# Performance work log

Hardware: AMD Instinct MI355X
Metric: run time of the kernel (lower is better)

Reference implementation:

```python
import jax, jax.numpy as jnp
import numpy as np

E, TWO_I, H = 8, 3072, 2048
I = TWO_I // 2
T = 16384

def setup_inputs() -> dict:
    key = jax.random.key(0)
    k1, k2, k3 = jax.random.split(key, 3)
    scale_gu = 1.0 / np.sqrt(H)
    scale_dn = 1.0 / np.sqrt(I)
    return {
        "current_state": jax.random.normal(k1, (T, H), dtype=jnp.float32),
        "gate_up_proj": jax.random.normal(k2, (E, TWO_I, H), dtype=jnp.float32) * scale_gu,
        "down_proj": jax.random.normal(k3, (E, H, I), dtype=jnp.float32) * scale_dn,
        "expert_idx": 3,
    }

def reference(current_state, gate_up_proj, down_proj, expert_idx):
    # F.linear(x, W) == x @ W.T
    w_gu = gate_up_proj[expert_idx]            # [2I, H]
    w_dn = down_proj[expert_idx]               # [H, I]
    gu = jnp.einsum("th,ih->ti", current_state, w_gu)  # [T, 2I]
    gate, up = jnp.split(gu, 2, axis=-1)       # each [T, I]
    hidden = jax.nn.silu(gate) * up            # SwiGLU gating
    return jnp.einsum("ti,hi->th", hidden, w_dn)  # [T, H]
```

## Files before the change

### kernel.cpp

```cpp
#include <hip/hip_runtime.h>
#include <hip/hip_bf16.h>


namespace {

constexpr int T_ = 16384;
constexpr int H_ = 2048;
constexpr int I_ = 1536;

typedef short short8 __attribute__((ext_vector_type(8)));
typedef float f32x4 __attribute__((ext_vector_type(4)));
typedef unsigned short ushort4v __attribute__((ext_vector_type(4)));

__device__ __forceinline__ unsigned short f2bf(float f) {
    union { float f; unsigned u; } v; v.f = f;
    return (unsigned short)((v.u + 0x7FFFu + ((v.u >> 16) & 1u)) >> 16);
}

typedef __attribute__((address_space(1))) const void gvoid;
typedef __attribute__((address_space(3))) void lvoid;
__device__ __forceinline__ void gload16(const void* g, void* l) {
    __builtin_amdgcn_global_load_lds((gvoid*)g, (lvoid*)l, 16, 0, 0);
}

__global__ void k_cvt_all(const float* __restrict__ x, const float* __restrict__ wgu,
                          const float* __restrict__ wdn, const int* __restrict__ eidx,
                          unsigned short* __restrict__ xb, unsigned short* __restrict__ wgub,
                          unsigned short* __restrict__ wdnb) {
    const int e = *eidx;
    const int n1 = T_ * H_ / 4;
    const int n2 = 2 * I_ * H_ / 4;
    const int n3 = H_ * I_ / 4;
    const int ntot = n1 + n2 + n3;
    const float* wgu_e = wgu + (size_t)e * (size_t)(2 * I_) * H_;
    const float* wdn_e = wdn + (size_t)e * (size_t)H_ * I_;
    const int stride = gridDim.x * blockDim.x;
    for (int i = blockIdx.x * blockDim.x + threadIdx.x; i < ntot; i += stride) {
        const float* src; unsigned short* dst; int j;
        if (i < n1)           { src = x;     dst = xb;   j = i; }
        else if (i < n1 + n2) { src = wgu_e; dst = wgub; j = i - n1; }
        else                  { src = wdn_e; dst = wdnb; j = i - n1 - n2; }
        f32x4 v = ((const f32x4*)src)[j];
        ushort4v h = { f2bf(v[0]), f2bf(v[1]), f2bf(v[2]), f2bf(v[3]) };
        ((ushort4v*)dst)[j] = h;
    }
}

__global__ __launch_bounds__(256, 2) void k_gemm1_swiglu(
    const unsigned short* __restrict__ xb, const unsigned short* __restrict__ wgub,
    unsigned short* __restrict__ hidden)
{
    __shared__ unsigned short lds[3 * 128 * 64];
    unsigned short* ldsA  = lds;
    unsigned short* ldsBg = lds + 128 * 64;
    unsigned short* ldsBu = lds + 2 * 128 * 64;

    const int tid  = threadIdx.x;
    const int lane = tid & 63;
    const int wv   = tid >> 6;
    const int wr   = wv >> 1, wc = wv & 1;

    const int nb = (blockIdx.x & 7) * 192 + (blockIdx.x >> 3);
    const int bx = nb % 12, by = nb / 12;
    const int m0 = by * 128;
    const int n0 = bx * 128;

    f32x4 accG[4][4], accU[4][4];
    #pragma unroll
    for (int a = 0; a < 4; ++a)
        #pragma unroll
        for (int b = 0; b < 4; ++b) { accG[a][b] = (f32x4)0.0f; accU[a][b] = (f32x4)0.0f; }

    const int drow = lane >> 3;
    const int gcol = (((lane & 7) ^ drow) * 8);
    const int l15 = lane & 15;
    const int l4  = lane >> 4;
    const int sw  = l15 & 7;

    for (int k0 = 0; k0 < H_; k0 += 64) {
        __syncthreads();
        #pragma unroll
        for (int r = 0; r < 4; ++r) {
            const int row  = r * 32 + wv * 8 + drow;
            const int loff = r * 2048 + wv * 512;
            gload16(xb   + (size_t)(m0 + row)      * H_ + k0 + gcol, ldsA  + loff);
            gload16(wgub + (size_t)(n0 + row)      * H_ + k0 + gcol, ldsBg + loff);
            gload16(wgub + (size_t)(I_ + n0 + row) * H_ + k0 + gcol, ldsBu + loff);
        }
        __syncthreads();

        #pragma unroll
        for (int kk = 0; kk < 2; ++kk) {
            const int sl = ((kk * 4 + l4) ^ sw) * 8;
            short8 af[4], bg[4], bu[4];
            #pragma unroll
            for (int a = 0; a < 4; ++a) {
                const int r = wr * 64 + a * 16 + l15;
                af[a] = *(const short8*)(ldsA + r * 64 + sl);
            }
            #pragma unroll
            for (int b = 0; b < 4; ++b) {
                const int r = wc * 64 + b * 16 + l15;
                bg[b] = *(const short8*)(ldsBg + r * 64 + sl);
                bu[b] = *(const short8*)(ldsBu + r * 64 + sl);
            }
            #pragma unroll
            for (int a = 0; a < 4; ++a)
                #pragma unroll
                for (int b = 0; b < 4; ++b) {
                    accG[a][b] = __builtin_amdgcn_mfma_f32_16x16x32_bf16(af[a], bg[b], accG[a][b], 0, 0, 0);
                    accU[a][b] = __builtin_amdgcn_mfma_f32_16x16x32_bf16(af[a], bu[b], accU[a][b], 0, 0, 0);
                }
        }
    }

    #pragma unroll
    for (int a = 0; a < 4; ++a)
        #pragma unroll
        for (int b = 0; b < 4; ++b)
            #pragma unroll
            for (int j = 0; j < 4; ++j) {
                const int row = m0 + wr * 64 + a * 16 + l4 * 4 + j;
                const int col = n0 + wc * 64 + b * 16 + l15;
                const float g = accG[a][b][j];
                const float u = accU[a][b][j];
                const float s = g / (1.0f + __expf(-g));
                hidden[(size_t)row * I_ + col] = f2bf(s * u);
            }
}

__global__ __launch_bounds__(256, 2) void k_gemm2(
    const unsigned short* __restrict__ hidden, const unsigned short* __restrict__ wdnb,
    float* __restrict__ out)
{
    __shared__ unsigned short lds[24576];
    unsigned short* ldsA = lds;
    unsigned short* ldsB = lds + 16384;

    const int tid  = threadIdx.x;
    const int lane = tid & 63;
    const int wv   = tid >> 6;
    const int wr   = wv >> 1;
    const int wc   = wv & 1;

    const int nb = (blockIdx.x & 7) * 128 + (blockIdx.x >> 3);
    const int bx = nb % 16, by = nb / 16;
    const int m0 = by * 256;
    const int n0 = bx * 128;

    f32x4 acc[8][4];
    #pragma unroll
    for (int a = 0; a < 8; ++a)
        #pragma unroll
        for (int b = 0; b < 4; ++b) acc[a][b] = (f32x4)0.0f;

    const int drow = lane >> 3;
    const int gcol = (((lane & 7) ^ drow) * 8);
    const int l15 = lane & 15;
    const int l4  = lane >> 4;
    const int sw  = l15 & 7;

    for (int k0 = 0; k0 < I_; k0 += 64) {
        __syncthreads();
        #pragma unroll
        for (int r = 0; r < 8; ++r) {
            const int row  = r * 32 + wv * 8 + drow;
            const int loff = r * 2048 + wv * 512;
            gload16(hidden + (size_t)(m0 + row) * I_ + k0 + gcol, ldsA + loff);
        }
        #pragma unroll
        for (int r = 0; r < 4; ++r) {
            const int row  = r * 32 + wv * 8 + drow;
            const int loff = r * 2048 + wv * 512;
            gload16(wdnb + (size_t)(n0 + row) * I_ + k0 + gcol, ldsB + loff);
        }
        __syncthreads();

        #pragma unroll
        for (int kk = 0; kk < 2; ++kk) {
            const int sl = ((kk * 4 + l4) ^ sw) * 8;
            short8 af[8], bw[4];
            #pragma unroll
            for (int a = 0; a < 8; ++a) {
                const int r = wr * 128 + a * 16 + l15;
                af[a] = *(const short8*)(ldsA + r * 64 + sl);
            }
            #pragma unroll
            for (int b = 0; b < 4; ++b) {
                const int r = wc * 64 + b * 16 + l15;
                bw[b] = *(const short8*)(ldsB + r * 64 + sl);
            }
            #pragma unroll
            for (int a = 0; a < 8; ++a)
                #pragma unroll
                for (int b = 0; b < 4; ++b)
                    acc[a][b] = __builtin_amdgcn_mfma_f32_16x16x32_bf16(af[a], bw[b], acc[a][b], 0, 0, 0);
        }
    }

    #pragma unroll
    for (int a = 0; a < 8; ++a)
        #pragma unroll
        for (int b = 0; b < 4; ++b)
            #pragma unroll
            for (int j = 0; j < 4; ++j) {
                const int row = m0 + wr * 128 + a * 16 + l4 * 4 + j;
                const int col = n0 + wc * 64 + b * 16 + l15;
                out[(size_t)row * H_ + col] = acc[a][b][j];
            }
}

}

extern "C" void kernel_launch(void* const* d_in, const int* in_sizes, int n_in,
                              void* d_out, int out_size, void* d_ws, size_t ws_size,
                              hipStream_t stream) {
    const float* x   = (const float*)d_in[0];
    const float* wgu = (const float*)d_in[1];
    const float* wdn = (const float*)d_in[2];
    const int* eidx  = (const int*)d_in[3];
    float* out = (float*)d_out;

    unsigned short* xb     = (unsigned short*)d_out;
    unsigned short* hidden = (unsigned short*)d_ws;
    unsigned short* wgub   = (unsigned short*)((char*)d_ws + 50331648);
    unsigned short* wdnb   = (unsigned short*)((char*)d_ws + 62914560);

    k_cvt_all<<<2048, 256, 0, stream>>>(x, wgu, wdn, eidx, xb, wgub, wdnb);
    k_gemm1_swiglu<<<dim3((I_ / 128) * (T_ / 128)), 256, 0, stream>>>(xb, wgub, hidden);
    k_gemm2<<<dim3((T_ / 256) * (H_ / 128)), 256, 0, stream>>>(hidden, wdnb, out);
}
```

Before: 324.2 us.

## Double-buffer activation tiles in both GEMMs and prefetch the next A tile

Both GEMM kernels now keep two LDS buffers for the activation (A) tile. The next k-step's A tile is issued with asynchronous global-to-LDS loads while the current step computes, and the wait uses explicit vmcnt counts in place of a full drain. The weight (B) tiles stay single-buffered and are loaded at the start of each step. The aim is to hide part of the global load latency behind MFMA work. The cost is more LDS per block (64KB and 80KB), which could limit occupancy at two blocks per CU, and the B loads are still exposed.

```diff
diff --git a/kernel.cpp b/kernel.cpp
--- a/kernel.cpp
+++ b/kernel.cpp
@@ -22,6 +22,9 @@
 __device__ __forceinline__ void gload16(const void* g, void* l) {
     __builtin_amdgcn_global_load_lds((gvoid*)g, (lvoid*)l, 16, 0, 0);
 }
+
+#define SBAR() do { __builtin_amdgcn_s_barrier(); __builtin_amdgcn_sched_barrier(0); } while (0)
+#define VMW(n) do { asm volatile("s_waitcnt vmcnt(" #n ")" ::: "memory"); __builtin_amdgcn_sched_barrier(0); } while (0)
 
 __global__ void k_cvt_all(const float* __restrict__ x, const float* __restrict__ wgu,
                           const float* __restrict__ wdn, const int* __restrict__ eidx,
@@ -50,10 +53,9 @@
     const unsigned short* __restrict__ xb, const unsigned short* __restrict__ wgub,
     unsigned short* __restrict__ hidden)
 {
-    __shared__ unsigned short lds[3 * 128 * 64];
-    unsigned short* ldsA  = lds;
-    unsigned short* ldsBg = lds + 128 * 64;
-    unsigned short* ldsBu = lds + 2 * 128 * 64;
+    __shared__ unsigned short lds[4 * 8192];
+    unsigned short* ldsBg = lds + 16384;
+    unsigned short* ldsBu = lds + 24576;
 
     const int tid  = threadIdx.x;
     const int lane = tid & 63;
@@ -77,18 +79,38 @@
     const int l4  = lane >> 4;
     const int sw  = l15 & 7;
 
-    for (int k0 = 0; k0 < H_; k0 += 64) {
-        __syncthreads();
+    constexpr int NT = H_ / 64;
+
+    auto stageA = [&](int t) {
+        unsigned short* dA = lds + (t & 1) * 8192;
+        const int kS = t * 64;
         #pragma unroll
         for (int r = 0; r < 4; ++r) {
             const int row  = r * 32 + wv * 8 + drow;
             const int loff = r * 2048 + wv * 512;
-            gload16(xb   + (size_t)(m0 + row)      * H_ + k0 + gcol, ldsA  + loff);
-            gload16(wgub + (size_t)(n0 + row)      * H_ + k0 + gcol, ldsBg + loff);
-            gload16(wgub + (size_t)(I_ + n0 + row) * H_ + k0 + gcol, ldsBu + loff);
-        }
-        __syncthreads();
-
+            gload16(xb + (size_t)(m0 + row) * H_ + kS + gcol, dA + loff);
+        }
+    };
+    auto stageB = [&](int t) {
+        const int kS = t * 64;
+        #pragma unroll
+        for (int r = 0; r < 4; ++r) {
+            const int row  = r * 32 + wv * 8 + drow;
+            const int loff = r * 2048 + wv * 512;
+            gload16(wgub + (size_t)(n0 + row)      * H_ + kS + gcol, ldsBg + loff);
+            gload16(wgub + (size_t)(I_ + n0 + row) * H_ + kS + gcol, ldsBu + loff);
+        }
+    };
+
+    stageA(0);
+
+    for (int t = 0; t < NT; ++t) {
+        stageB(t);
+        if (t + 1 < NT) { stageA(t + 1); VMW(4); }
+        else            { VMW(0); }
+        SBAR();
+
+        const unsigned short* bA = lds + (t & 1) * 8192;
         #pragma unroll
         for (int kk = 0; kk < 2; ++kk) {
             const int sl = ((kk * 4 + l4) ^ sw) * 8;
@@ -96,7 +118,7 @@
             #pragma unroll
             for (int a = 0; a < 4; ++a) {
                 const int r = wr * 64 + a * 16 + l15;
-                af[a] = *(const short8*)(ldsA + r * 64 + sl);
+                af[a] = *(const short8*)(bA + r * 64 + sl);
             }
             #pragma unroll
             for (int b = 0; b < 4; ++b) {
@@ -112,6 +134,7 @@
                     accU[a][b] = __builtin_amdgcn_mfma_f32_16x16x32_bf16(af[a], bu[b], accU[a][b], 0, 0, 0);
                 }
         }
+        SBAR();
     }
 
     #pragma unroll
@@ -133,9 +156,8 @@
     const unsigned short* __restrict__ hidden, const unsigned short* __restrict__ wdnb,
     float* __restrict__ out)
 {
-    __shared__ unsigned short lds[24576];
-    unsigned short* ldsA = lds;
-    unsigned short* ldsB = lds + 16384;
+    __shared__ unsigned short lds[2 * 16384 + 8192];
+    unsigned short* ldsB = lds + 32768;
 
     const int tid  = threadIdx.x;
     const int lane = tid & 63;
@@ -160,22 +182,37 @@
     const int l4  = lane >> 4;
     const int sw  = l15 & 7;
 
-    for (int k0 = 0; k0 < I_; k0 += 64) {
-        __syncthreads();
+    constexpr int NT = I_ / 64;
+
+    auto stageA = [&](int t) {
+        unsigned short* dA = lds + (t & 1) * 16384;
+        const int kS = t * 64;
         #pragma unroll
         for (int r = 0; r < 8; ++r) {
             const int row  = r * 32 + wv * 8 + drow;
             const int loff = r * 2048 + wv * 512;
-            gload16(hidden + (size_t)(m0 + row) * I_ + k0 + gcol, ldsA + loff);
-        }
+            gload16(hidden + (size_t)(m0 + row) * I_ + kS + gcol, dA + loff);
+        }
+    };
+    auto stageB = [&](int t) {
+        const int kS = t * 64;
         #pragma unroll
         for (int r = 0; r < 4; ++r) {
             const int row  = r * 32 + wv * 8 + drow;
             const int loff = r * 2048 + wv * 512;
-            gload16(wdnb + (size_t)(n0 + row) * I_ + k0 + gcol, ldsB + loff);
-        }
-        __syncthreads();
-
+            gload16(wdnb + (size_t)(n0 + row) * I_ + kS + gcol, ldsB + loff);
+        }
+    };
+
+    stageA(0);
+
+    for (int t = 0; t < NT; ++t) {
+        stageB(t);
+        if (t + 1 < NT) { stageA(t + 1); VMW(8); }
+        else            { VMW(0); }
+        SBAR();
+
+        const unsigned short* bA = lds + (t & 1) * 16384;
         #pragma unroll
         for (int kk = 0; kk < 2; ++kk) {
             const int sl = ((kk * 4 + l4) ^ sw) * 8;
@@ -183,7 +220,7 @@
             #pragma unroll
             for (int a = 0; a < 8; ++a) {
                 const int r = wr * 128 + a * 16 + l15;
-                af[a] = *(const short8*)(ldsA + r * 64 + sl);
+                af[a] = *(const short8*)(bA + r * 64 + sl);
             }
             #pragma unroll
             for (int b = 0; b < 4; ++b) {
@@ -196,6 +233,7 @@
                 for (int b = 0; b < 4; ++b)
                     acc[a][b] = __builtin_amdgcn_mfma_f32_16x16x32_bf16(af[a], bw[b], acc[a][b], 0, 0, 0);
         }
+        SBAR();
     }
 
     #pragma unroll
```

New measurement: 319.4 us. Within noise of the previous version (-1.5%).

## Double-buffer gate/up weight tiles in GEMM1 with explicit vmcnt waits

Applied to the files above, without the earlier changes.

Splits GEMM1 tile staging into a single-buffered activation load and a double-buffered gate/up weight load. The next k-step's weight tiles are prefetched while the current step runs its MFMAs, and a partial `s_waitcnt vmcnt(8)` plus raw barriers replace the two full `__syncthreads` per iteration. The aim is to hide global-to-LDS latency for the weight tiles. In exchange, LDS use per block grows from 48KB to 80KB, which may limit occupancy. The activation tile still has to finish loading before compute each step.

```diff
diff --git a/kernel.cpp b/kernel.cpp
--- a/kernel.cpp
+++ b/kernel.cpp
@@ -22,6 +22,9 @@
 __device__ __forceinline__ void gload16(const void* g, void* l) {
     __builtin_amdgcn_global_load_lds((gvoid*)g, (lvoid*)l, 16, 0, 0);
 }
+
+#define SBAR() do { __builtin_amdgcn_s_barrier(); __builtin_amdgcn_sched_barrier(0); } while (0)
+#define VMW(n) do { asm volatile("s_waitcnt vmcnt(" #n ")" ::: "memory"); __builtin_amdgcn_sched_barrier(0); } while (0)
 
 __global__ void k_cvt_all(const float* __restrict__ x, const float* __restrict__ wgu,
                           const float* __restrict__ wdn, const int* __restrict__ eidx,
@@ -50,10 +53,10 @@
     const unsigned short* __restrict__ xb, const unsigned short* __restrict__ wgub,
     unsigned short* __restrict__ hidden)
 {
-    __shared__ unsigned short lds[3 * 128 * 64];
+    __shared__ unsigned short lds[5 * 8192];
     unsigned short* ldsA  = lds;
-    unsigned short* ldsBg = lds + 128 * 64;
-    unsigned short* ldsBu = lds + 2 * 128 * 64;
+    unsigned short* ldsBg = lds + 8192;
+    unsigned short* ldsBu = lds + 24576;
 
     const int tid  = threadIdx.x;
     const int lane = tid & 63;
@@ -77,18 +80,40 @@
     const int l4  = lane >> 4;
     const int sw  = l15 & 7;
 
-    for (int k0 = 0; k0 < H_; k0 += 64) {
-        __syncthreads();
+    constexpr int NT = H_ / 64;
+
+    auto stageA = [&](int t) {
+        const int kS = t * 64;
         #pragma unroll
         for (int r = 0; r < 4; ++r) {
             const int row  = r * 32 + wv * 8 + drow;
             const int loff = r * 2048 + wv * 512;
-            gload16(xb   + (size_t)(m0 + row)      * H_ + k0 + gcol, ldsA  + loff);
-            gload16(wgub + (size_t)(n0 + row)      * H_ + k0 + gcol, ldsBg + loff);
-            gload16(wgub + (size_t)(I_ + n0 + row) * H_ + k0 + gcol, ldsBu + loff);
-        }
-        __syncthreads();
-
+            gload16(xb + (size_t)(m0 + row) * H_ + kS + gcol, ldsA + loff);
+        }
+    };
+    auto stageB = [&](int t) {
+        unsigned short* dBg = ldsBg + (t & 1) * 8192;
+        unsigned short* dBu = ldsBu + (t & 1) * 8192;
+        const int kS = t * 64;
+        #pragma unroll
+        for (int r = 0; r < 4; ++r) {
+            const int row  = r * 32 + wv * 8 + drow;
+            const int loff = r * 2048 + wv * 512;
+            gload16(wgub + (size_t)(n0 + row)      * H_ + kS + gcol, dBg + loff);
+            gload16(wgub + (size_t)(I_ + n0 + row) * H_ + kS + gcol, dBu + loff);
+        }
+    };
+
+    stageB(0);
+
+    for (int t = 0; t < NT; ++t) {
+        stageA(t);
+        if (t + 1 < NT) { stageB(t + 1); VMW(8); }
+        else            { VMW(0); }
+        SBAR();
+
+        const unsigned short* bBg = ldsBg + (t & 1) * 8192;
+        const unsigned short* bBu = ldsBu + (t & 1) * 8192;
         #pragma unroll
         for (int kk = 0; kk < 2; ++kk) {
             const int sl = ((kk * 4 + l4) ^ sw) * 8;
@@ -101,8 +126,8 @@
             #pragma unroll
             for (int b = 0; b < 4; ++b) {
                 const int r = wc * 64 + b * 16 + l15;
-                bg[b] = *(const short8*)(ldsBg + r * 64 + sl);
-                bu[b] = *(const short8*)(ldsBu + r * 64 + sl);
+                bg[b] = *(const short8*)(bBg + r * 64 + sl);
+                bu[b] = *(const short8*)(bBu + r * 64 + sl);
             }
             #pragma unroll
             for (int a = 0; a < 4; ++a)
@@ -112,6 +137,7 @@
                     accU[a][b] = __builtin_amdgcn_mfma_f32_16x16x32_bf16(af[a], bu[b], accU[a][b], 0, 0, 0);
                 }
         }
+        SBAR();
     }
 
     #pragma unroll
```

Result: no change. 328.3 us (+1.3%).
